# Kernel optimization log

Hardware: AMD Instinct MI355X
Metric: run time of the kernel (lower is better)

Reference implementation:

```python
import jax, jax.numpy as jnp
import numpy as np

B, T, C, H = 8, 2048, 1024, 128  # batch, seq (== block_size), embed dim, head size


def setup_inputs() -> dict:
    key = jax.random.key(0)
    kx, kq, kk, kv = jax.random.split(key, 4)
    x = jax.random.normal(kx, (B, T, C), dtype=jnp.float32)
    # torch Linear(no bias) weights: [head_size, in_features], applied as x @ W.T
    s = 1.0 / np.sqrt(C)
    Wq = jax.random.normal(kq, (H, C), dtype=jnp.float32) * s
    Wk = jax.random.normal(kk, (H, C), dtype=jnp.float32) * s
    Wv = jax.random.normal(kv, (H, C), dtype=jnp.float32) * s
    return {"x": x, "Wq": Wq, "Wk": Wk, "Wv": Wv}


def reference(x, Wq, Wk, Wv):
    # projections: [B,T,C] @ [C,H] -> [B,T,H]
    q = jnp.einsum('btc,hc->bth', x, Wq)
    k = jnp.einsum('btc,hc->bth', x, Wk)
    v = jnp.einsum('btc,hc->bth', x, Wv)
    scale = k.shape[-1] ** -0.5
    # scores [B,T,T], causal mask, softmax in fp32 (autocast disabled in original)
    scores = jnp.einsum('bqh,bkh->bqk', q, k) * scale
    causal = jnp.tril(jnp.ones((T, T), dtype=bool))
    scores = jnp.where(causal, scores, -jnp.inf)
    attn = jax.nn.softmax(scores.astype(jnp.float32), axis=-1)
    # dropout_rate = 0.0 -> identity
    out = jnp.einsum('bqk,bkh->bqh', attn.astype(v.dtype), v)
    return out
```

## Files before the change

kernel.cpp:

```cpp
#include <hip/hip_runtime.h>
#include <hip/hip_bf16.h>

constexpr int NB = 8;
constexpr int T  = 2048;
constexpr int C  = 1024;
constexpr int Hd = 128;

typedef short bf16x8 __attribute__((ext_vector_type(8)));
typedef float floatx4 __attribute__((ext_vector_type(4)));

__device__ __forceinline__ ushort f2bf(float x) {
    return __builtin_bit_cast(ushort, __float2bfloat16(x));
}
__device__ __forceinline__ float bf2f(ushort u) {
    unsigned int x = ((unsigned int)u) << 16;
    return __builtin_bit_cast(float, x);
}
__device__ __forceinline__ void async16(ushort* lds, const ushort* g) {
    __builtin_amdgcn_global_load_lds(
        (const __attribute__((address_space(1))) unsigned int*)g,
        (__attribute__((address_space(3))) unsigned int*)lds, 16, 0, 0);
}

__global__ __launch_bounds__(256) void convert_xw(
    const float* __restrict__ X, const float* __restrict__ Wq,
    const float* __restrict__ Wk, const float* __restrict__ Wv,
    ushort* __restrict__ Xb, ushort* __restrict__ Wb)
{
    int bid = blockIdx.x;
    if (bid < 8192) {
        size_t i = ((size_t)bid * 256 + threadIdx.x) * 8;
        float4 a = *(const float4*)&X[i];
        float4 b = *(const float4*)&X[i + 4];
        bf16x8 o;
        o[0] = (short)f2bf(a.x); o[1] = (short)f2bf(a.y);
        o[2] = (short)f2bf(a.z); o[3] = (short)f2bf(a.w);
        o[4] = (short)f2bf(b.x); o[5] = (short)f2bf(b.y);
        o[6] = (short)f2bf(b.z); o[7] = (short)f2bf(b.w);
        *(bf16x8*)&Xb[i] = o;
    } else {
        int g = (bid - 8192) * 256 + threadIdx.x;
        size_t base = (size_t)g * 8;
        int sel = (int)(base >> 17);
        const float* W = sel == 0 ? Wq : (sel == 1 ? Wk : Wv);
        float s = (sel == 0) ? 0.12751744f : 1.0f;
        size_t off = base - (size_t)sel * 131072;
        float4 a = *(const float4*)&W[off];
        float4 b = *(const float4*)&W[off + 4];
        bf16x8 o;
        o[0] = (short)f2bf(a.x * s); o[1] = (short)f2bf(a.y * s);
        o[2] = (short)f2bf(a.z * s); o[3] = (short)f2bf(a.w * s);
        o[4] = (short)f2bf(b.x * s); o[5] = (short)f2bf(b.y * s);
        o[6] = (short)f2bf(b.z * s); o[7] = (short)f2bf(b.w * s);
        *(bf16x8*)&Wb[base] = o;
    }
}

__global__ __launch_bounds__(256) void qkv_gemm(
    const ushort* __restrict__ Xb, const ushort* __restrict__ Wb,
    ushort* __restrict__ Qo, ushort* __restrict__ Ko, ushort* __restrict__ Vt)
{
    __shared__ ushort SM[12288];
    ushort* Al = SM;
    ushort* Bl = SM + 8192;
    const int m0 = blockIdx.x * 128;
    const int n0 = blockIdx.y * 64;
    const int tid = threadIdx.x, lane = tid & 63, wave = tid >> 6;
    const int quad = lane >> 4, colL = lane & 15;
    const int wm = (wave & 1) * 64, wn = (wave >> 1) * 32;
    const int lr = lane >> 3;
    const int lcs = ((lane & 7) ^ (lr & 7)) * 8;

    floatx4 acc[4][2] = {};

    for (int k0 = 0; k0 < C; k0 += 64) {
        for (int t = 0; t < 4; ++t) {
            int q = wave * 4 + t;
            async16(&Al[q * 512 + lane * 8],
                    &Xb[(size_t)(m0 + q * 8 + lr) * C + k0 + lcs]);
        }
        for (int t = 0; t < 2; ++t) {
            int q = wave * 2 + t;
            async16(&Bl[q * 512 + lane * 8],
                    &Wb[(size_t)(n0 + q * 8 + lr) * C + k0 + lcs]);
        }
        __syncthreads();

        bf16x8 af[2][4], bfr[2][2];
        for (int kk = 0; kk < 2; ++kk) {
            for (int mt = 0; mt < 4; ++mt)
                af[kk][mt] = *(const bf16x8*)
                    &Al[(wm + mt * 16 + colL) * 64 + (((kk * 4 + quad) ^ (colL & 7))) * 8];
            for (int nt = 0; nt < 2; ++nt)
                bfr[kk][nt] = *(const bf16x8*)
                    &Bl[(wn + nt * 16 + colL) * 64 + (((kk * 4 + quad) ^ (colL & 7))) * 8];
        }
        for (int kk = 0; kk < 2; ++kk)
            for (int mt = 0; mt < 4; ++mt)
                for (int nt = 0; nt < 2; ++nt)
                    acc[mt][nt] = __builtin_amdgcn_mfma_f32_16x16x32_bf16(
                        af[kk][mt], bfr[kk][nt], acc[mt][nt], 0, 0, 0);
        __syncthreads();
    }

    const int sel = n0 >> 7;
    const int h0 = n0 & 127;
    if (sel < 2) {
        ushort* dst = sel == 0 ? Qo : Ko;
        for (int mt = 0; mt < 4; ++mt)
            for (int nt = 0; nt < 2; ++nt)
                for (int r = 0; r < 4; ++r) {
                    int row = m0 + wm + mt * 16 + quad * 4 + r;
                    int h = h0 + wn + nt * 16 + colL;
                    dst[(size_t)row * Hd + h] = f2bf(acc[mt][nt][r]);
                }
    } else {
        ushort* TL = SM;
        for (int mt = 0; mt < 4; ++mt)
            for (int nt = 0; nt < 2; ++nt)
                for (int r = 0; r < 4; ++r)
                    TL[(wm + mt * 16 + quad * 4 + r) * 66 + wn + nt * 16 + colL] =
                        f2bf(acc[mt][nt][r]);
        __syncthreads();
        const int b = m0 >> 11, tb = m0 & 2047;
        const int h = tid & 63, tq = tid >> 6;
        for (int st = 0; st < 4; ++st) {
            int t0 = tq * 32 + st * 8;
            bf16x8 o;
            for (int jx = 0; jx < 8; ++jx)
                o[jx] = (short)TL[(t0 + jx) * 66 + h];
            *(bf16x8*)&Vt[((size_t)b * Hd + h0 + h) * T + tb + t0] = o;
        }
    }
}

__global__ __launch_bounds__(256, 2) void attn_partial(
    const ushort* __restrict__ Q, const ushort* __restrict__ Kg,
    const ushort* __restrict__ Vt, ushort* __restrict__ Opart,
    float* __restrict__ mpart, float* __restrict__ lpart)
{
    __shared__ ushort Kl[128 * 128];
    __shared__ ushort Vl[128 * 128];

    const int tid = threadIdx.x, lane = tid & 63, wave = tid >> 6;
    const int quad = lane >> 4, colL = lane & 15;

    int id = blockIdx.x;
    int b = id / 136;
    int rem = id - b * 136;
    int j = 15;
    while (rem >= j + 1) { rem -= (j + 1); --j; }
    int c = rem;
    const int q0 = j * 128;
    const int k0 = c * 128;
    const bool diag = (c == j);

    {
        int r = tid >> 4, p = tid & 15;
        for (int t = 0; t < 8; ++t) {
            int row = t * 16 + r;
            async16(&Kl[t * 2048 + tid * 8],
                    &Kg[((size_t)b * T + k0 + row) * Hd + ((p ^ (row & 15)) * 8)]);
        }
        for (int t = 0; t < 8; ++t) {
            int hrow = t * 16 + r;
            async16(&Vl[t * 2048 + tid * 8],
                    &Vt[((size_t)b * Hd + hrow) * T + k0 + ((p ^ (hrow & 15)) * 8)]);
        }
    }

    bf16x8 qa[2][4];
    for (int mi = 0; mi < 2; ++mi) {
        const ushort* qp =
            &Q[((size_t)b * T + q0 + wave * 32 + mi * 16 + colL) * Hd + quad * 8];
        for (int ks = 0; ks < 4; ++ks)
            qa[mi][ks] = *(const bf16x8*)&qp[ks * 32];
    }

    __syncthreads();

    floatx4 accS[2][8] = {};
    for (int ks = 0; ks < 4; ++ks)
        for (int nt = 0; nt < 8; ++nt) {
            int krow = nt * 16 + colL;
            bf16x8 kb = *(const bf16x8*)&Kl[krow * 128 + (((ks * 4 + quad) ^ colL) * 8)];
            accS[0][nt] = __builtin_amdgcn_mfma_f32_16x16x32_bf16(qa[0][ks], kb, accS[0][nt], 0, 0, 0);
            accS[1][nt] = __builtin_amdgcn_mfma_f32_16x16x32_bf16(qa[1][ks], kb, accS[1][nt], 0, 0, 0);
        }

    if (diag) {
        for (int mi = 0; mi < 2; ++mi)
            for (int nt = 0; nt < 8; ++nt)
                for (int rr = 0; rr < 4; ++rr) {
                    int lrow = wave * 32 + mi * 16 + quad * 4 + rr;
                    int lcol = nt * 16 + colL;
                    if (lcol > lrow) accS[mi][nt][rr] = -__builtin_inff();
                }
    }
    __syncthreads();

    ushort* Pw = &Kl[wave * 4096];
    float m_r[2][4], l_r[2][4];
    for (int mi = 0; mi < 2; ++mi)
        for (int rr = 0; rr < 4; ++rr) {
            float mx = accS[mi][0][rr];
            for (int nt = 1; nt < 8; ++nt) mx = fmaxf(mx, accS[mi][nt][rr]);
            for (int off = 1; off < 16; off <<= 1)
                mx = fmaxf(mx, __shfl_xor(mx, off, 64));
            m_r[mi][rr] = mx;
            l_r[mi][rr] = 0.f;
        }
    for (int mi = 0; mi < 2; ++mi) {
        for (int nt = 0; nt < 8; ++nt)
            for (int rr = 0; rr < 4; ++rr) {
                float p = __builtin_amdgcn_exp2f(accS[mi][nt][rr] - m_r[mi][rr]);
                l_r[mi][rr] += p;
                int prow = mi * 16 + quad * 4 + rr;
                Pw[prow * 128 + ((nt * 16 + colL) ^ ((prow & 7) << 4))] = f2bf(p);
            }
        for (int rr = 0; rr < 4; ++rr) {
            float s = l_r[mi][rr];
            for (int off = 1; off < 16; off <<= 1)
                s += __shfl_xor(s, off, 64);
            l_r[mi][rr] = s;
        }
    }

    bf16x8 pa[2][4];
    for (int mi = 0; mi < 2; ++mi) {
        int prow = mi * 16 + colL;
        int sw = (prow & 7) << 4;
        for (int ks = 0; ks < 4; ++ks)
            pa[mi][ks] = *(const bf16x8*)&Pw[prow * 128 + ((ks * 32 + quad * 8) ^ sw)];
    }

    floatx4 Oacc[2][8] = {};
    for (int ks = 0; ks < 4; ++ks)
        for (int th = 0; th < 8; ++th) {
            int hrow = th * 16 + colL;
            bf16x8 vb = *(const bf16x8*)&Vl[hrow * 128 + (((ks * 4 + quad) ^ colL) * 8)];
            Oacc[0][th] = __builtin_amdgcn_mfma_f32_16x16x32_bf16(pa[0][ks], vb, Oacc[0][th], 0, 0, 0);
            Oacc[1][th] = __builtin_amdgcn_mfma_f32_16x16x32_bf16(pa[1][ks], vb, Oacc[1][th], 0, 0, 0);
        }

    const int slot = b * 136 + (j * (j + 1)) / 2 + c;
    ushort* Op = &Opart[(size_t)slot * 16384];
    for (int mi = 0; mi < 2; ++mi)
        for (int th = 0; th < 8; ++th)
            for (int rr = 0; rr < 4; ++rr) {
                int row = wave * 32 + mi * 16 + quad * 4 + rr;
                Op[row * 128 + th * 16 + colL] = f2bf(Oacc[mi][th][rr]);
            }
    if (colL == 0)
        for (int mi = 0; mi < 2; ++mi)
            for (int rr = 0; rr < 4; ++rr) {
                int row = wave * 32 + mi * 16 + quad * 4 + rr;
                mpart[(size_t)slot * 128 + row] = m_r[mi][rr];
                lpart[(size_t)slot * 128 + row] = l_r[mi][rr];
            }
}

__global__ __launch_bounds__(256) void attn_combine(
    const ushort* __restrict__ Opart, const float* __restrict__ mpart,
    const float* __restrict__ lpart, float* __restrict__ out)
{
    const int j = blockIdx.x, b = blockIdx.y;
    const int nch = j + 1;
    const int sbase = b * 136 + (j * (j + 1)) / 2;
    const int t = threadIdx.x;
    const int row = blockIdx.z * 32 + (t >> 3);
    const int h0 = (t & 7) * 16;

    float M = -__builtin_inff();
    for (int c = 0; c < nch; ++c)
        M = fmaxf(M, mpart[(size_t)(sbase + c) * 128 + row]);
    float ltot = 0.f;
    for (int c = 0; c < nch; ++c)
        ltot += lpart[(size_t)(sbase + c) * 128 + row] *
                __builtin_amdgcn_exp2f(mpart[(size_t)(sbase + c) * 128 + row] - M);

    float o[16];
    for (int i = 0; i < 16; ++i) o[i] = 0.f;
    for (int c = 0; c < nch; ++c) {
        float wgt = __builtin_amdgcn_exp2f(mpart[(size_t)(sbase + c) * 128 + row] - M);
        const ushort* Op = &Opart[(size_t)(sbase + c) * 16384 + row * 128 + h0];
        for (int x = 0; x < 2; ++x) {
            bf16x8 v = *(const bf16x8*)&Op[x * 8];
            for (int i2 = 0; i2 < 8; ++i2)
                o[x * 8 + i2] += bf2f((ushort)v[i2]) * wgt;
        }
    }
    float inv = 1.0f / ltot;
    float* dst = &out[((size_t)(b * T) + j * 128 + row) * Hd + h0];
    for (int i = 0; i < 16; ++i) dst[i] = o[i] * inv;
}

extern "C" void kernel_launch(void* const* d_in, const int* in_sizes, int n_in,
                              void* d_out, int out_size, void* d_ws, size_t ws_size,
                              hipStream_t stream) {
    const float* x  = (const float*)d_in[0];
    const float* Wq = (const float*)d_in[1];
    const float* Wk = (const float*)d_in[2];
    const float* Wv = (const float*)d_in[3];
    float* out = (float*)d_out;

    char* w = (char*)d_ws;
    ushort* Xb = (ushort*)w;
    ushort* Wb = (ushort*)(w + (size_t)33554432);
    ushort* Opart = (ushort*)w;
    float* mpart = (float*)(w + (size_t)35651584);
    float* lpart = (float*)(w + (size_t)35651584 + 557056);
    w += (size_t)35651584 + 2 * 557056;
    ushort* Qb  = (ushort*)w;  w += (size_t)NB * T * Hd * 2;
    ushort* Kb  = (ushort*)w;  w += (size_t)NB * T * Hd * 2;
    ushort* Vtb = (ushort*)w;  w += (size_t)NB * T * Hd * 2;

    convert_xw<<<8384, 256, 0, stream>>>(x, Wq, Wk, Wv, Xb, Wb);
    qkv_gemm<<<dim3(128, 6), 256, 0, stream>>>(Xb, Wb, Qb, Kb, Vtb);
    attn_partial<<<1088, 256, 0, stream>>>(Qb, Kb, Vtb, Opart, mpart, lpart);
    attn_combine<<<dim3(16, 8, 4), 256, 0, stream>>>(Opart, mpart, lpart, out);
}
```

Baseline: 162.8 us.

## Swap MFMA operands to get transposed accumulators and pack bf16 stores

Swaps the MFMA operand order in the QKV GEMM and attention kernels, so each lane's accumulator holds four consecutive columns of one row. Outputs can then be written as packed 8-byte bf16 stores instead of scalar 2-byte stores. Row max and sum reductions now need only two cross-lane shuffles, and P goes through a separate per-wave LDS buffer in two halves, which removes a __syncthreads. The combine kernel launches the largest query blocks first. The risk is higher LDS usage from the added P buffer, which could lower occupancy.

```diff
diff --git a/kernel.cpp b/kernel.cpp
--- a/kernel.cpp
+++ b/kernel.cpp
@@ -15,6 +15,9 @@
 __device__ __forceinline__ float bf2f(ushort u) {
     unsigned int x = ((unsigned int)u) << 16;
     return __builtin_bit_cast(float, x);
+}
+__device__ __forceinline__ unsigned pk2(float a, float b) {
+    return ((unsigned)f2bf(a)) | (((unsigned)f2bf(b)) << 16);
 }
 __device__ __forceinline__ void async16(ushort* lds, const ushort* g) {
     __builtin_amdgcn_global_load_lds(
@@ -71,7 +74,7 @@
     const int lr = lane >> 3;
     const int lcs = ((lane & 7) ^ (lr & 7)) * 8;
 
-    floatx4 acc[4][2] = {};
+    floatx4 accT[2][4] = {};
 
     for (int k0 = 0; k0 < C; k0 += 64) {
         for (int t = 0; t < 4; ++t) {
@@ -96,10 +99,10 @@
                     &Bl[(wn + nt * 16 + colL) * 64 + (((kk * 4 + quad) ^ (colL & 7))) * 8];
         }
         for (int kk = 0; kk < 2; ++kk)
-            for (int mt = 0; mt < 4; ++mt)
-                for (int nt = 0; nt < 2; ++nt)
-                    acc[mt][nt] = __builtin_amdgcn_mfma_f32_16x16x32_bf16(
-                        af[kk][mt], bfr[kk][nt], acc[mt][nt], 0, 0, 0);
+            for (int nt = 0; nt < 2; ++nt)
+                for (int mt = 0; mt < 4; ++mt)
+                    accT[nt][mt] = __builtin_amdgcn_mfma_f32_16x16x32_bf16(
+                        bfr[kk][nt], af[kk][mt], accT[nt][mt], 0, 0, 0);
         __syncthreads();
     }
 
@@ -107,20 +110,26 @@
     const int h0 = n0 & 127;
     if (sel < 2) {
         ushort* dst = sel == 0 ? Qo : Ko;
-        for (int mt = 0; mt < 4; ++mt)
-            for (int nt = 0; nt < 2; ++nt)
-                for (int r = 0; r < 4; ++r) {
-                    int row = m0 + wm + mt * 16 + quad * 4 + r;
-                    int h = h0 + wn + nt * 16 + colL;
-                    dst[(size_t)row * Hd + h] = f2bf(acc[mt][nt][r]);
-                }
+        for (int nt = 0; nt < 2; ++nt)
+            for (int mt = 0; mt < 4; ++mt) {
+                int row = m0 + wm + mt * 16 + colL;
+                int h = h0 + wn + nt * 16 + quad * 4;
+                uint2 pk;
+                pk.x = pk2(accT[nt][mt][0], accT[nt][mt][1]);
+                pk.y = pk2(accT[nt][mt][2], accT[nt][mt][3]);
+                *(uint2*)&dst[(size_t)row * Hd + h] = pk;
+            }
     } else {
         ushort* TL = SM;
-        for (int mt = 0; mt < 4; ++mt)
-            for (int nt = 0; nt < 2; ++nt)
-                for (int r = 0; r < 4; ++r)
-                    TL[(wm + mt * 16 + quad * 4 + r) * 66 + wn + nt * 16 + colL] =
-                        f2bf(acc[mt][nt][r]);
+        for (int nt = 0; nt < 2; ++nt)
+            for (int mt = 0; mt < 4; ++mt) {
+                int t = wm + mt * 16 + colL;
+                int h = wn + nt * 16 + quad * 4;
+                uint2 pk;
+                pk.x = pk2(accT[nt][mt][0], accT[nt][mt][1]);
+                pk.y = pk2(accT[nt][mt][2], accT[nt][mt][3]);
+                *(uint2*)&TL[t * 68 + h] = pk;
+            }
         __syncthreads();
         const int b = m0 >> 11, tb = m0 & 2047;
         const int h = tid & 63, tq = tid >> 6;
@@ -128,7 +137,7 @@
             int t0 = tq * 32 + st * 8;
             bf16x8 o;
             for (int jx = 0; jx < 8; ++jx)
-                o[jx] = (short)TL[(t0 + jx) * 66 + h];
+                o[jx] = (short)TL[(t0 + jx) * 68 + h];
             *(bf16x8*)&Vt[((size_t)b * Hd + h0 + h) * T + tb + t0] = o;
         }
     }
@@ -141,6 +150,7 @@
 {
     __shared__ ushort Kl[128 * 128];
     __shared__ ushort Vl[128 * 128];
+    __shared__ ushort Pl[4][2048];
 
     const int tid = threadIdx.x, lane = tid & 63, wave = tid >> 6;
     const int quad = lane >> 4, colL = lane & 15;
@@ -170,101 +180,116 @@
     }
 
     bf16x8 qa[2][4];
-    for (int mi = 0; mi < 2; ++mi) {
+    for (int qg = 0; qg < 2; ++qg) {
         const ushort* qp =
-            &Q[((size_t)b * T + q0 + wave * 32 + mi * 16 + colL) * Hd + quad * 8];
+            &Q[((size_t)b * T + q0 + wave * 32 + qg * 16 + colL) * Hd + quad * 8];
         for (int ks = 0; ks < 4; ++ks)
-            qa[mi][ks] = *(const bf16x8*)&qp[ks * 32];
+            qa[qg][ks] = *(const bf16x8*)&qp[ks * 32];
     }
 
     __syncthreads();
 
-    floatx4 accS[2][8] = {};
+    floatx4 accST[2][8] = {};
     for (int ks = 0; ks < 4; ++ks)
-        for (int nt = 0; nt < 8; ++nt) {
-            int krow = nt * 16 + colL;
-            bf16x8 kb = *(const bf16x8*)&Kl[krow * 128 + (((ks * 4 + quad) ^ colL) * 8)];
-            accS[0][nt] = __builtin_amdgcn_mfma_f32_16x16x32_bf16(qa[0][ks], kb, accS[0][nt], 0, 0, 0);
-            accS[1][nt] = __builtin_amdgcn_mfma_f32_16x16x32_bf16(qa[1][ks], kb, accS[1][nt], 0, 0, 0);
+        for (int kt = 0; kt < 8; ++kt) {
+            bf16x8 kb = *(const bf16x8*)
+                &Kl[(kt * 16 + colL) * 128 + (((ks * 4 + quad) ^ colL) * 8)];
+            accST[0][kt] = __builtin_amdgcn_mfma_f32_16x16x32_bf16(
+                kb, qa[0][ks], accST[0][kt], 0, 0, 0);
+            accST[1][kt] = __builtin_amdgcn_mfma_f32_16x16x32_bf16(
+                kb, qa[1][ks], accST[1][kt], 0, 0, 0);
         }
 
     if (diag) {
-        for (int mi = 0; mi < 2; ++mi)
-            for (int nt = 0; nt < 8; ++nt)
+        for (int qg = 0; qg < 2; ++qg) {
+            int qglob = q0 + wave * 32 + qg * 16 + colL;
+            for (int kt = 0; kt < 8; ++kt)
                 for (int rr = 0; rr < 4; ++rr) {
-                    int lrow = wave * 32 + mi * 16 + quad * 4 + rr;
-                    int lcol = nt * 16 + colL;
-                    if (lcol > lrow) accS[mi][nt][rr] = -__builtin_inff();
+                    int keyg = k0 + kt * 16 + quad * 4 + rr;
+                    if (keyg > qglob) accST[qg][kt][rr] = -__builtin_inff();
                 }
-    }
-    __syncthreads();
-
-    ushort* Pw = &Kl[wave * 4096];
-    float m_r[2][4], l_r[2][4];
-    for (int mi = 0; mi < 2; ++mi)
-        for (int rr = 0; rr < 4; ++rr) {
-            float mx = accS[mi][0][rr];
-            for (int nt = 1; nt < 8; ++nt) mx = fmaxf(mx, accS[mi][nt][rr]);
-            for (int off = 1; off < 16; off <<= 1)
-                mx = fmaxf(mx, __shfl_xor(mx, off, 64));
-            m_r[mi][rr] = mx;
-            l_r[mi][rr] = 0.f;
-        }
-    for (int mi = 0; mi < 2; ++mi) {
-        for (int nt = 0; nt < 8; ++nt)
-            for (int rr = 0; rr < 4; ++rr) {
-                float p = __builtin_amdgcn_exp2f(accS[mi][nt][rr] - m_r[mi][rr]);
-                l_r[mi][rr] += p;
-                int prow = mi * 16 + quad * 4 + rr;
-                Pw[prow * 128 + ((nt * 16 + colL) ^ ((prow & 7) << 4))] = f2bf(p);
-            }
-        for (int rr = 0; rr < 4; ++rr) {
-            float s = l_r[mi][rr];
-            for (int off = 1; off < 16; off <<= 1)
-                s += __shfl_xor(s, off, 64);
-            l_r[mi][rr] = s;
-        }
-    }
-
-    bf16x8 pa[2][4];
-    for (int mi = 0; mi < 2; ++mi) {
-        int prow = mi * 16 + colL;
-        int sw = (prow & 7) << 4;
-        for (int ks = 0; ks < 4; ++ks)
-            pa[mi][ks] = *(const bf16x8*)&Pw[prow * 128 + ((ks * 32 + quad * 8) ^ sw)];
-    }
-
-    floatx4 Oacc[2][8] = {};
-    for (int ks = 0; ks < 4; ++ks)
-        for (int th = 0; th < 8; ++th) {
-            int hrow = th * 16 + colL;
-            bf16x8 vb = *(const bf16x8*)&Vl[hrow * 128 + (((ks * 4 + quad) ^ colL) * 8)];
-            Oacc[0][th] = __builtin_amdgcn_mfma_f32_16x16x32_bf16(pa[0][ks], vb, Oacc[0][th], 0, 0, 0);
-            Oacc[1][th] = __builtin_amdgcn_mfma_f32_16x16x32_bf16(pa[1][ks], vb, Oacc[1][th], 0, 0, 0);
-        }
+        }
+    }
+
+    float m_r[2], l_r[2];
+    for (int qg = 0; qg < 2; ++qg) {
+        float mx = accST[qg][0][0];
+        for (int kt = 0; kt < 8; ++kt)
+            for (int rr = 0; rr < 4; ++rr)
+                mx = fmaxf(mx, accST[qg][kt][rr]);
+        mx = fmaxf(mx, __shfl_xor(mx, 16, 64));
+        mx = fmaxf(mx, __shfl_xor(mx, 32, 64));
+        m_r[qg] = mx;
+        l_r[qg] = 0.f;
+    }
+
+    ushort* Plw = Pl[wave];
+    floatx4 OaccT[2][8] = {};
+    for (int kh = 0; kh < 2; ++kh) {
+        for (int qg = 0; qg < 2; ++qg) {
+            int q = qg * 16 + colL;
+            for (int ktl = 0; ktl < 4; ++ktl) {
+                floatx4 sv = accST[qg][kh * 4 + ktl];
+                float p0 = __builtin_amdgcn_exp2f(sv[0] - m_r[qg]);
+                float p1 = __builtin_amdgcn_exp2f(sv[1] - m_r[qg]);
+                float p2 = __builtin_amdgcn_exp2f(sv[2] - m_r[qg]);
+                float p3 = __builtin_amdgcn_exp2f(sv[3] - m_r[qg]);
+                l_r[qg] += (p0 + p1) + (p2 + p3);
+                int chunk = ktl * 2 + (quad >> 1);
+                uint2 pk;
+                pk.x = pk2(p0, p1);
+                pk.y = pk2(p2, p3);
+                *(uint2*)&Plw[q * 64 + ((chunk ^ (q & 7)) * 8) + (quad & 1) * 4] = pk;
+            }
+        }
+        for (int ksl = 0; ksl < 2; ++ksl) {
+            int ks = kh * 2 + ksl;
+            bf16x8 pf[2];
+            for (int qg = 0; qg < 2; ++qg) {
+                int q = qg * 16 + colL;
+                pf[qg] = *(const bf16x8*)
+                    &Plw[q * 64 + (((ksl * 4 + quad) ^ (q & 7)) * 8)];
+            }
+            for (int mh = 0; mh < 8; ++mh) {
+                bf16x8 vb = *(const bf16x8*)
+                    &Vl[(mh * 16 + colL) * 128 + (((ks * 4 + quad) ^ colL) * 8)];
+                OaccT[0][mh] = __builtin_amdgcn_mfma_f32_16x16x32_bf16(
+                    vb, pf[0], OaccT[0][mh], 0, 0, 0);
+                OaccT[1][mh] = __builtin_amdgcn_mfma_f32_16x16x32_bf16(
+                    vb, pf[1], OaccT[1][mh], 0, 0, 0);
+            }
+        }
+    }
+
+    for (int qg = 0; qg < 2; ++qg) {
+        float s = l_r[qg];
+        s += __shfl_xor(s, 16, 64);
+        s += __shfl_xor(s, 32, 64);
+        l_r[qg] = s;
+    }
 
     const int slot = b * 136 + (j * (j + 1)) / 2 + c;
     ushort* Op = &Opart[(size_t)slot * 16384];
-    for (int mi = 0; mi < 2; ++mi)
-        for (int th = 0; th < 8; ++th)
-            for (int rr = 0; rr < 4; ++rr) {
-                int row = wave * 32 + mi * 16 + quad * 4 + rr;
-                Op[row * 128 + th * 16 + colL] = f2bf(Oacc[mi][th][rr]);
-            }
-    if (colL == 0)
-        for (int mi = 0; mi < 2; ++mi)
-            for (int rr = 0; rr < 4; ++rr) {
-                int row = wave * 32 + mi * 16 + quad * 4 + rr;
-                mpart[(size_t)slot * 128 + row] = m_r[mi][rr];
-                lpart[(size_t)slot * 128 + row] = l_r[mi][rr];
-            }
+    for (int qg = 0; qg < 2; ++qg) {
+        int q = wave * 32 + qg * 16 + colL;
+        for (int mh = 0; mh < 8; ++mh) {
+            uint2 pk;
+            pk.x = pk2(OaccT[qg][mh][0], OaccT[qg][mh][1]);
+            pk.y = pk2(OaccT[qg][mh][2], OaccT[qg][mh][3]);
+            *(uint2*)&Op[q * 128 + mh * 16 + quad * 4] = pk;
+        }
+        if (quad == 0) {
+            mpart[(size_t)slot * 128 + q] = m_r[qg];
+            lpart[(size_t)slot * 128 + q] = l_r[qg];
+        }
+    }
 }
 
 __global__ __launch_bounds__(256) void attn_combine(
     const ushort* __restrict__ Opart, const float* __restrict__ mpart,
     const float* __restrict__ lpart, float* __restrict__ out)
 {
-    const int j = blockIdx.x, b = blockIdx.y;
+    const int j = 15 - blockIdx.x, b = blockIdx.y;
     const int nch = j + 1;
     const int sbase = b * 136 + (j * (j + 1)) / 2;
     const int t = threadIdx.x;
```

Result: slower. 166.9 us (+2.5%).
